# Kernel tuning notes

Hardware: AMD Instinct MI355X
Metric: run time of the kernel (lower is better)

Reference implementation:

```python
import jax, jax.numpy as jnp
import numpy as np

T, C, N, H = 60, 128, 4096, 128  # timesteps, channels(=hidden), pixel samples, hidden
GP = 5  # gp_affected_timesteps


def setup_inputs() -> dict:
    key = jax.random.key(0)
    k1, k2, k3 = jax.random.split(key, 3)
    s = 1.0 / np.sqrt(H)
    return {
        "image_stack": jax.random.normal(k1, (T, C, N), dtype=jnp.float32),
        "mask": jnp.zeros((T, N), dtype=jnp.float32),  # accepted but unused by original forward
        "W_ih": jax.random.uniform(k2, (4 * H, C), dtype=jnp.float32, minval=-s, maxval=s),
        "W_hh": jax.random.uniform(k3, (4 * H, H), dtype=jnp.float32, minval=-s, maxval=s),
        "b_ih": jnp.zeros((4 * H,), dtype=jnp.float32),
        "b_hh": jnp.zeros((4 * H,), dtype=jnp.float32),
        "gp_affected_timesteps": GP,
    }


def _lstm_cell(carry, xt, W_ih, W_hh, b):
    h, c = carry
    gates = xt @ W_ih.T + h @ W_hh.T + b  # [N, 4H]
    i, f, g, o = jnp.split(gates, 4, axis=-1)
    i, f, o = jax.nn.sigmoid(i), jax.nn.sigmoid(f), jax.nn.sigmoid(o)
    g = jnp.tanh(g)
    c = f * c + i * g
    h = o * jnp.tanh(c)
    return (h, c), h


def reference(image_stack, mask, W_ih, W_hh, b_ih, b_hh, gp_affected_timesteps):
    t, ch, n = image_stack.shape
    h = ch  # output fed back as input => hidden == channels
    b = b_ih + b_hh
    xs = jnp.transpose(image_stack, (0, 2, 1))  # [T, N, C]
    init = (jnp.zeros((n, h), image_stack.dtype), jnp.zeros((n, h), image_stack.dtype))

    cell = lambda carry, xt: _lstm_cell(carry, xt, W_ih, W_hh, b)
    carry, outs1 = jax.lax.scan(cell, init, xs)  # [T, N, H]

    extra = t - gp_affected_timesteps - 1
    ar = lambda carry, _: _lstm_cell(carry, carry[0], W_ih, W_hh, b)
    carry, outs2 = jax.lax.scan(ar, carry, None, length=extra)  # [extra, N, H]

    outs = jnp.concatenate([outs1, outs2], axis=0)  # [T+extra, N, H]
    return jnp.transpose(outs, (1, 0, 2))  # batch-first [N, T+extra, H]
```

## Files before the change

### kernel.cpp

```cpp
#include <hip/hip_runtime.h>
#include <hip/hip_bf16.h>

typedef __attribute__((ext_vector_type(8))) short short8;
typedef __attribute__((ext_vector_type(4))) float f32x4;

constexpr int T    = 60;
constexpr int C    = 128;
constexpr int NPIX = 4096;
constexpr int H    = 128;
constexpr int GP   = 5;
constexpr int EXTRA = T - GP - 1;
constexpr int TT    = T + EXTRA;
constexpr int LDS_STRIDE = 136;

__device__ __forceinline__ unsigned short f2bf(float f) {
  unsigned u = __float_as_uint(f);
  u += 0x7FFF + ((u >> 16) & 1);
  return (unsigned short)(u >> 16);
}
__device__ __forceinline__ float bf2f(unsigned short s) {
  return __uint_as_float(((unsigned)s) << 16);
}
__device__ __forceinline__ float fast_sigmoid(float x) {
  float e = __builtin_amdgcn_exp2f(-1.44269504f * x);
  return __builtin_amdgcn_rcpf(1.0f + e);
}
__device__ __forceinline__ float fast_tanh(float x) {
  float e = __builtin_amdgcn_exp2f(2.88539008f * x);
  return 1.0f - 2.0f * __builtin_amdgcn_rcpf(1.0f + e);
}

__global__ __launch_bounds__(512, 2) void lstm_persistent(
    const float* __restrict__ img,
    const float* __restrict__ wih,
    const float* __restrict__ whh,
    const float* __restrict__ bih,
    const float* __restrict__ bhh,
    float* __restrict__ out)
{
  __shared__ __align__(16) unsigned short xs[16 * LDS_STRIDE];
  __shared__ __align__(16) unsigned short hs[16 * LDS_STRIDE];

  const int tid  = threadIdx.x;
  const int lane = tid & 63;
  const int w    = tid >> 6;
  const int l15  = lane & 15;
  const int quad = lane >> 4;
  const int n0   = blockIdx.x * 16;
  const int hid  = w * 16 + l15;

  short8 fih[4][4], fhh[4][4];
  float bias[4];
  #pragma unroll
  for (int nt = 0; nt < 4; ++nt) {
    const int col = nt * 128 + hid;
    bias[nt] = bih[col] + bhh[col];
    #pragma unroll
    for (int kt = 0; kt < 4; ++kt) {
      const int k0 = kt * 32 + quad * 8;
      const float* pih = wih + col * C + k0;
      const float* phh = whh + col * C + k0;
      short8 a, b;
      #pragma unroll
      for (int j = 0; j < 8; ++j) {
        a[j] = (short)f2bf(pih[j]);
        b[j] = (short)f2bf(phh[j]);
      }
      fih[nt][kt] = a;
      fhh[nt][kt] = b;
    }
  }

  for (int i = tid; i < 16 * LDS_STRIDE; i += 512) hs[i] = 0;

  float c[4] = {0.f, 0.f, 0.f, 0.f};

  const int nl = tid & 15;
  const int cb = (tid >> 4) * 4;
  const float* xbase = img + (size_t)cb * NPIX + n0 + nl;

  {
    float p0 = xbase[0], p1 = xbase[NPIX], p2 = xbase[2 * NPIX], p3 = xbase[3 * NPIX];
    ushort4 pk;
    pk.x = f2bf(p0); pk.y = f2bf(p1); pk.z = f2bf(p2); pk.w = f2bf(p3);
    *(ushort4*)&xs[nl * LDS_STRIDE + cb] = pk;
  }
  __syncthreads();

  const int fro = l15 * LDS_STRIDE + quad * 8;

  for (int t = 0; t < TT; ++t) {
    const bool pf = (t + 1 < T);
    float q0, q1, q2, q3;
    if (pf) {
      const float* p = xbase + (size_t)(t + 1) * C * NPIX;
      q0 = p[0]; q1 = p[NPIX]; q2 = p[2 * NPIX]; q3 = p[3 * NPIX];
    }

    if (t == T) {
      #pragma unroll
      for (int nt = 0; nt < 4; ++nt)
        #pragma unroll
        for (int kt = 0; kt < 4; ++kt) {
          short8 a = fih[nt][kt], b = fhh[nt][kt];
          #pragma unroll
          for (int j = 0; j < 8; ++j)
            a[j] = (short)f2bf(bf2f((unsigned short)a[j]) + bf2f((unsigned short)b[j]));
          fih[nt][kt] = a;
        }
    }

    f32x4 acc[4];
    #pragma unroll
    for (int nt = 0; nt < 4; ++nt)
      acc[nt] = (f32x4){bias[nt], bias[nt], bias[nt], bias[nt]};

    if (t < T) {
      #pragma unroll
      for (int kt = 0; kt < 4; ++kt) {
        short8 ax = *(const short8*)&xs[fro + kt * 32];
        short8 ah = *(const short8*)&hs[fro + kt * 32];
        #pragma unroll
        for (int nt = 0; nt < 4; ++nt) {
          acc[nt] = __builtin_amdgcn_mfma_f32_16x16x32_bf16(ax, fih[nt][kt], acc[nt], 0, 0, 0);
          acc[nt] = __builtin_amdgcn_mfma_f32_16x16x32_bf16(ah, fhh[nt][kt], acc[nt], 0, 0, 0);
        }
      }
    } else {
      #pragma unroll
      for (int kt = 0; kt < 4; ++kt) {
        short8 ah = *(const short8*)&hs[fro + kt * 32];
        #pragma unroll
        for (int nt = 0; nt < 4; ++nt)
          acc[nt] = __builtin_amdgcn_mfma_f32_16x16x32_bf16(ah, fih[nt][kt], acc[nt], 0, 0, 0);
      }
    }

    float hv[4];
    #pragma unroll
    for (int r = 0; r < 4; ++r) {
      float ig = fast_sigmoid(acc[0][r]);
      float fg = fast_sigmoid(acc[1][r]);
      float gg = fast_tanh(acc[2][r]);
      float og = fast_sigmoid(acc[3][r]);
      c[r] = fg * c[r] + ig * gg;
      hv[r] = og * fast_tanh(c[r]);
    }

    {
      float* ob = out + (size_t)(n0 + quad * 4) * (TT * H) + (size_t)t * H + hid;
      #pragma unroll
      for (int r = 0; r < 4; ++r)
        __builtin_nontemporal_store(hv[r], ob + (size_t)r * (TT * H));
    }

    __syncthreads();

    if (pf) {
      ushort4 pk;
      pk.x = f2bf(q0); pk.y = f2bf(q1); pk.z = f2bf(q2); pk.w = f2bf(q3);
      *(ushort4*)&xs[nl * LDS_STRIDE + cb] = pk;
    }
    #pragma unroll
    for (int r = 0; r < 4; ++r)
      hs[(quad * 4 + r) * LDS_STRIDE + hid] = f2bf(hv[r]);

    __syncthreads();
  }
}

extern "C" void kernel_launch(void* const* d_in, const int* in_sizes, int n_in,
                              void* d_out, int out_size, void* d_ws, size_t ws_size,
                              hipStream_t stream) {
  (void)in_sizes; (void)n_in; (void)d_ws; (void)ws_size; (void)out_size;
  const float* img = (const float*)d_in[0];
  const float* wih = (const float*)d_in[2];
  const float* whh = (const float*)d_in[3];
  const float* bih = (const float*)d_in[4];
  const float* bhh = (const float*)d_in[5];
  float* out = (float*)d_out;

  lstm_persistent<<<NPIX / 16, 512, 0, stream>>>(img, wih, whh, bih, bhh, out);
}
```

Baseline: 427.6 us.

## Double-buffer x/h LDS tiles to use one barrier per LSTM step

Makes the xs and hs shared-memory tiles ping-pong buffers, so each step reads one buffer and writes the next. This drops the second __syncthreads per timestep and uses a lighter custom barrier (lgkmcnt wait plus s_barrier). The loop is also split into a driven phase and an autoregressive phase, unrolled by two with x prefetched two steps ahead, which removes per-step branches. LDS usage doubles and the prefetch keeps more values live in registers.

After: 526.5 us. 1.23x slower.

```diff
diff --git a/kernel.cpp b/kernel.cpp
--- a/kernel.cpp
+++ b/kernel.cpp
@@ -12,6 +12,7 @@
 constexpr int EXTRA = T - GP - 1;
 constexpr int TT    = T + EXTRA;
 constexpr int LDS_STRIDE = 136;
+constexpr int BUFE = 16 * LDS_STRIDE;
 
 __device__ __forceinline__ unsigned short f2bf(float f) {
   unsigned u = __float_as_uint(f);
@@ -28,6 +29,12 @@
 __device__ __forceinline__ float fast_tanh(float x) {
   float e = __builtin_amdgcn_exp2f(2.88539008f * x);
   return 1.0f - 2.0f * __builtin_amdgcn_rcpf(1.0f + e);
+}
+
+__device__ __forceinline__ void wg_barrier() {
+  asm volatile("s_waitcnt lgkmcnt(0)" ::: "memory");
+  __builtin_amdgcn_s_barrier();
+  __builtin_amdgcn_sched_barrier(0);
 }
 
 __global__ __launch_bounds__(512, 2) void lstm_persistent(
@@ -38,8 +45,8 @@
     const float* __restrict__ bhh,
     float* __restrict__ out)
 {
-  __shared__ __align__(16) unsigned short xs[16 * LDS_STRIDE];
-  __shared__ __align__(16) unsigned short hs[16 * LDS_STRIDE];
+  __shared__ __align__(16) unsigned short xs[2 * BUFE];
+  __shared__ __align__(16) unsigned short hs[2 * BUFE];
 
   const int tid  = threadIdx.x;
   const int lane = tid & 63;
@@ -71,7 +78,7 @@
     }
   }
 
-  for (int i = tid; i < 16 * LDS_STRIDE; i += 512) hs[i] = 0;
+  for (int i = tid; i < BUFE; i += 512) hs[i] = 0;
 
   float c[4] = {0.f, 0.f, 0.f, 0.f};
 
@@ -79,63 +86,44 @@
   const int cb = (tid >> 4) * 4;
   const float* xbase = img + (size_t)cb * NPIX + n0 + nl;
 
+  auto loadx = [&](int t) -> f32x4 {
+    const float* p = xbase + (size_t)t * (C * NPIX);
+    return (f32x4){p[0], p[NPIX], p[2 * NPIX], p[3 * NPIX]};
+  };
+
   {
-    float p0 = xbase[0], p1 = xbase[NPIX], p2 = xbase[2 * NPIX], p3 = xbase[3 * NPIX];
+    f32x4 q = loadx(0);
     ushort4 pk;
-    pk.x = f2bf(p0); pk.y = f2bf(p1); pk.z = f2bf(p2); pk.w = f2bf(p3);
+    pk.x = f2bf(q[0]); pk.y = f2bf(q[1]); pk.z = f2bf(q[2]); pk.w = f2bf(q[3]);
     *(ushort4*)&xs[nl * LDS_STRIDE + cb] = pk;
   }
-  __syncthreads();
+  f32x4 qcur = loadx(1);
+  wg_barrier();
 
   const int fro = l15 * LDS_STRIDE + quad * 8;
-
-  for (int t = 0; t < TT; ++t) {
-    const bool pf = (t + 1 < T);
-    float q0, q1, q2, q3;
-    if (pf) {
-      const float* p = xbase + (size_t)(t + 1) * C * NPIX;
-      q0 = p[0]; q1 = p[NPIX]; q2 = p[2 * NPIX]; q3 = p[3 * NPIX];
-    }
-
-    if (t == T) {
-      #pragma unroll
-      for (int nt = 0; nt < 4; ++nt)
-        #pragma unroll
-        for (int kt = 0; kt < 4; ++kt) {
-          short8 a = fih[nt][kt], b = fhh[nt][kt];
-          #pragma unroll
-          for (int j = 0; j < 8; ++j)
-            a[j] = (short)f2bf(bf2f((unsigned short)a[j]) + bf2f((unsigned short)b[j]));
-          fih[nt][kt] = a;
-        }
-    }
-
+  float* ob = out + (size_t)(n0 + quad * 4) * (TT * H) + hid;
+  const size_t obs = (size_t)TT * H;
+
+  auto step_drv = [&](int so, int dso, bool wx, f32x4 qx) {
     f32x4 acc[4];
     #pragma unroll
     for (int nt = 0; nt < 4; ++nt)
       acc[nt] = (f32x4){bias[nt], bias[nt], bias[nt], bias[nt]};
-
-    if (t < T) {
-      #pragma unroll
-      for (int kt = 0; kt < 4; ++kt) {
-        short8 ax = *(const short8*)&xs[fro + kt * 32];
-        short8 ah = *(const short8*)&hs[fro + kt * 32];
-        #pragma unroll
-        for (int nt = 0; nt < 4; ++nt) {
-          acc[nt] = __builtin_amdgcn_mfma_f32_16x16x32_bf16(ax, fih[nt][kt], acc[nt], 0, 0, 0);
-          acc[nt] = __builtin_amdgcn_mfma_f32_16x16x32_bf16(ah, fhh[nt][kt], acc[nt], 0, 0, 0);
-        }
+    #pragma unroll
+    for (int kt = 0; kt < 4; ++kt) {
+      short8 ax = *(const short8*)&xs[so + fro + kt * 32];
+      short8 ah = *(const short8*)&hs[so + fro + kt * 32];
+      #pragma unroll
+      for (int nt = 0; nt < 4; ++nt) {
+        acc[nt] = __builtin_amdgcn_mfma_f32_16x16x32_bf16(ax, fih[nt][kt], acc[nt], 0, 0, 0);
+        acc[nt] = __builtin_amdgcn_mfma_f32_16x16x32_bf16(ah, fhh[nt][kt], acc[nt], 0, 0, 0);
       }
-    } else {
-      #pragma unroll
-      for (int kt = 0; kt < 4; ++kt) {
-        short8 ah = *(const short8*)&hs[fro + kt * 32];
-        #pragma unroll
-        for (int nt = 0; nt < 4; ++nt)
-          acc[nt] = __builtin_amdgcn_mfma_f32_16x16x32_bf16(ah, fih[nt][kt], acc[nt], 0, 0, 0);
-      }
-    }
-
+    }
+    if (wx) {
+      ushort4 pk;
+      pk.x = f2bf(qx[0]); pk.y = f2bf(qx[1]); pk.z = f2bf(qx[2]); pk.w = f2bf(qx[3]);
+      *(ushort4*)&xs[dso + nl * LDS_STRIDE + cb] = pk;
+    }
     float hv[4];
     #pragma unroll
     for (int r = 0; r < 4; ++r) {
@@ -146,26 +134,83 @@
       c[r] = fg * c[r] + ig * gg;
       hv[r] = og * fast_tanh(c[r]);
     }
-
-    {
-      float* ob = out + (size_t)(n0 + quad * 4) * (TT * H) + (size_t)t * H + hid;
-      #pragma unroll
-      for (int r = 0; r < 4; ++r)
-        __builtin_nontemporal_store(hv[r], ob + (size_t)r * (TT * H));
-    }
-
-    __syncthreads();
-
-    if (pf) {
-      ushort4 pk;
-      pk.x = f2bf(q0); pk.y = f2bf(q1); pk.z = f2bf(q2); pk.w = f2bf(q3);
-      *(ushort4*)&xs[nl * LDS_STRIDE + cb] = pk;
-    }
-    #pragma unroll
-    for (int r = 0; r < 4; ++r)
-      hs[(quad * 4 + r) * LDS_STRIDE + hid] = f2bf(hv[r]);
-
-    __syncthreads();
+    #pragma unroll
+    for (int r = 0; r < 4; ++r)
+      hs[dso + (quad * 4 + r) * LDS_STRIDE + hid] = f2bf(hv[r]);
+    #pragma unroll
+    for (int r = 0; r < 4; ++r)
+      __builtin_nontemporal_store(hv[r], ob + (size_t)r * obs);
+    ob += H;
+    wg_barrier();
+  };
+
+  auto step_ar = [&](int so, int dso) {
+    f32x4 acc[4];
+    #pragma unroll
+    for (int nt = 0; nt < 4; ++nt)
+      acc[nt] = (f32x4){bias[nt], bias[nt], bias[nt], bias[nt]};
+    #pragma unroll
+    for (int kt = 0; kt < 4; ++kt) {
+      short8 ah = *(const short8*)&hs[so + fro + kt * 32];
+      #pragma unroll
+      for (int nt = 0; nt < 4; ++nt)
+        acc[nt] = __builtin_amdgcn_mfma_f32_16x16x32_bf16(ah, fih[nt][kt], acc[nt], 0, 0, 0);
+    }
+    float hv[4];
+    #pragma unroll
+    for (int r = 0; r < 4; ++r) {
+      float ig = fast_sigmoid(acc[0][r]);
+      float fg = fast_sigmoid(acc[1][r]);
+      float gg = fast_tanh(acc[2][r]);
+      float og = fast_sigmoid(acc[3][r]);
+      c[r] = fg * c[r] + ig * gg;
+      hv[r] = og * fast_tanh(c[r]);
+    }
+    #pragma unroll
+    for (int r = 0; r < 4; ++r)
+      hs[dso + (quad * 4 + r) * LDS_STRIDE + hid] = f2bf(hv[r]);
+    #pragma unroll
+    for (int r = 0; r < 4; ++r)
+      __builtin_nontemporal_store(hv[r], ob + (size_t)r * obs);
+    ob += H;
+    wg_barrier();
+  };
+
+  #pragma unroll 1
+  for (int t = 0; t < T - 4; t += 2) {
+    f32x4 qA = loadx(t + 2);
+    step_drv(0, BUFE, true, qcur);
+    f32x4 qB = loadx(t + 3);
+    step_drv(BUFE, 0, true, qA);
+    qcur = qB;
+  }
+  {
+    f32x4 qA = loadx(58);
+    step_drv(0, BUFE, true, qcur);
+    f32x4 qB = loadx(59);
+    step_drv(BUFE, 0, true, qA);
+    qcur = qB;
+  }
+  {
+    step_drv(0, BUFE, true, qcur);
+    step_drv(BUFE, 0, false, qcur);
+  }
+
+  #pragma unroll
+  for (int nt = 0; nt < 4; ++nt)
+    #pragma unroll
+    for (int kt = 0; kt < 4; ++kt) {
+      short8 a = fih[nt][kt], b = fhh[nt][kt];
+      #pragma unroll
+      for (int j = 0; j < 8; ++j)
+        a[j] = (short)f2bf(bf2f((unsigned short)a[j]) + bf2f((unsigned short)b[j]));
+      fih[nt][kt] = a;
+    }
+
+  #pragma unroll 1
+  for (int t = 0; t < EXTRA; t += 2) {
+    step_ar(0, BUFE);
+    step_ar(BUFE, 0);
   }
 }
 
```
